# Optimization experiments

Measured on AMD Instinct MI355X. Metric: run time of the kernel, lower is better.

## Reference

```python
import jax, jax.numpy as jnp
import numpy as np

N_NODES = 100000
N_EDGES = 800000


def setup_inputs() -> dict:
    key = jax.random.key(0)
    ks = jax.random.split(key, 8)
    s = 0.05  # weight scale
    return {
        "x": jax.random.normal(ks[0], (N_NODES, 64), dtype=jnp.float32),
        "edge_index": jax.random.randint(ks[1], (2, N_EDGES), 0, N_NODES, dtype=jnp.int64),
        "eps1": jnp.zeros((), jnp.float32),
        "eps2": jnp.zeros((), jnp.float32),
        "W1a": jax.random.normal(ks[2], (64, 128), dtype=jnp.float32) * s,
        "b1a": jnp.zeros((128,), jnp.float32),
        "W1b": jax.random.normal(ks[3], (128, 128), dtype=jnp.float32) * s,
        "b1b": jnp.zeros((128,), jnp.float32),
        "W2a": jax.random.normal(ks[4], (128, 128), dtype=jnp.float32) * s,
        "b2a": jnp.zeros((128,), jnp.float32),
        "W2b": jax.random.normal(ks[5], (128, 64), dtype=jnp.float32) * s,
        "b2b": jnp.zeros((64,), jnp.float32),
    }


def _gin_conv(h, src, dst, eps, Wa, ba, Wb, bb, n_nodes):
    # sum-aggregate neighbor messages h[src] at dst, add (1+eps)*self
    agg = jax.ops.segment_sum(h[src], dst, num_segments=n_nodes)  # [N, d]
    z = (1.0 + eps) * h + agg
    # MLP: Linear -> ReLU -> Linear (weights stored [in, out])
    return jnp.maximum(z @ Wa + ba, 0.0) @ Wb + bb


def reference(x, edge_index, eps1, eps2, W1a, b1a, W1b, b1b, W2a, b2a, W2b, b2b):
    src, dst = edge_index[0], edge_index[1]
    n = x.shape[0]
    h = _gin_conv(x, src, dst, eps1, W1a, b1a, W1b, b1b, n)
    h = jnp.maximum(h, 0.0)  # outer ReLU; dropout is identity in eval
    out = _gin_conv(h, src, dst, eps2, W2a, b2a, W2b, b2b, n)
    return out
```

## Files before the change

kernel.cpp:

```cpp
#include <hip/hip_runtime.h>
#include <cstdint>

constexpr int CAP = 32;
constexpr int FIX = 16;

typedef __attribute__((ext_vector_type(8))) __bf16 bf16x8;
typedef __attribute__((ext_vector_type(16))) float f32x16;

__device__ __forceinline__ unsigned short f2bf(float f) {
    unsigned int u = __builtin_bit_cast(unsigned int, f);
    u += 0x7fffu + ((u >> 16) & 1u);
    return (unsigned short)(u >> 16);
}
__device__ __forceinline__ float bf2f(unsigned short h) {
    unsigned int u = ((unsigned int)h) << 16;
    return __builtin_bit_cast(float, u);
}


__global__ void init_kernel(int* __restrict__ counts, int N,
                            const float* __restrict__ W1a, const float* __restrict__ W1b,
                            const float* __restrict__ W2a, const float* __restrict__ W2b,
                            unsigned short* __restrict__ wpk) {
    int i = blockIdx.x * 256 + threadIdx.x;
    if (i < N) counts[i] = 0;
    if (i < 49152) {
        const float* W;
        int K, Nn, base, rel;
        if (i < 8192) {
            W = W1a; K = 64; Nn = 128; base = 0; rel = i;
        } else if (i < 24576) {
            W = W1b; K = 128; Nn = 128; base = 16384; rel = i - 8192;
        } else if (i < 40960) {
            W = W2a; K = 128; Nn = 128; base = 49152; rel = i - 24576;
        } else {
            W = W2b; K = 128; Nn = 64; base = 81920; rel = i - 40960;
        }
        int j = rel & 7;
        int lane = (rel >> 3) & 63;
        int rest = rel >> 9;
        int ksteps = K / 16;
        int kstep = rest % ksteps;
        int ntile = rest / ksteps;
        int k = kstep * 16 + ((lane >> 5) << 3) + j;
        int ncol = ntile * 32 + (lane & 31);
        float v = W[k * Nn + ncol];
        unsigned short h = f2bf(v);
        unsigned short l = f2bf(v - bf2f(h));
        wpk[base + rel] = h;
        wpk[base + K * Nn + rel] = l;
    }
}


__global__ void bucket_kernel(const int* __restrict__ eidx, int E,
                              int* __restrict__ counts, int* __restrict__ buckets) {
    int e = blockIdx.x * 256 + threadIdx.x;
    if (e < E) {
        int d = eidx[E + e];
        int pos = atomicAdd(&counts[d], 1);
        if (pos < CAP) buckets[(size_t)d * CAP + pos] = eidx[e];
    }
}


template <int KIN, int KMID, int KOUT, bool RELU_OUT>
__global__ __launch_bounds__(512, 8) void gin_layer_kernel(
    const float* __restrict__ h, const int* __restrict__ cnts, const int* __restrict__ buckets,
    const float* __restrict__ eps,
    const unsigned short* __restrict__ Wahi, const unsigned short* __restrict__ Walo,
    const float* __restrict__ ba,
    const unsigned short* __restrict__ Wbhi, const unsigned short* __restrict__ Wblo,
    const float* __restrict__ bb, float* __restrict__ out, int n) {
    constexpr int ZS = KIN + 8;
    constexpr int TS = KMID + 8;
    constexpr int KSB = KIN / 16;
    constexpr int KSC = KMID / 16;
    __shared__ __align__(16) unsigned short smem[2 * 64 * (KMID + 8)];
    unsigned short* const zhi = smem;
    unsigned short* const zlo = smem + 64 * ZS;
    unsigned short* const thi = smem;
    unsigned short* const tlo = smem + 64 * TS;

    const int tid = threadIdx.x;
    const int lane = tid & 63;
    const int base = blockIdx.x * 64;
    const float scale = 1.0f + eps[0];
    const int wq = __builtin_amdgcn_readfirstlane(tid >> 6);

    float h0x, h0y;
    if (KIN == 64) {
        h0x = h[lane];
        h0y = 0.f;
    } else {
        const float2* h2 = (const float2*)h;
        float2 t0 = h2[lane];
        h0x = t0.x;
        h0y = t0.y;
    }

#pragma unroll
    for (int mi = 0; mi < 8; ++mi) {
        const int m = wq * 8 + mi;
        const int node = base + m;
        const int nc = node < n ? node : n - 1;
        const int cl0 = __builtin_amdgcn_readfirstlane(cnts[nc]);
        const int cl = cl0 < CAP ? cl0 : CAP;
        const int* __restrict__ srcs = buckets + (size_t)nc * CAP;

        int sIdx[FIX];
#pragma unroll
        for (int j = 0; j < FIX; ++j) {
            int sj = srcs[j];
            sIdx[j] = j < cl ? sj : 0;
        }

        if (KIN == 64) {
            float a0 = 0.f, a1 = 0.f, a2 = 0.f, a3 = 0.f;
            float a4 = 0.f, a5 = 0.f, a6 = 0.f, a7 = 0.f;
#pragma unroll
            for (int j = 0; j < FIX; j += 8) {
                a0 += h[(size_t)sIdx[j + 0] * 64 + lane];
                a1 += h[(size_t)sIdx[j + 1] * 64 + lane];
                a2 += h[(size_t)sIdx[j + 2] * 64 + lane];
                a3 += h[(size_t)sIdx[j + 3] * 64 + lane];
                a4 += h[(size_t)sIdx[j + 4] * 64 + lane];
                a5 += h[(size_t)sIdx[j + 5] * 64 + lane];
                a6 += h[(size_t)sIdx[j + 6] * 64 + lane];
                a7 += h[(size_t)sIdx[j + 7] * 64 + lane];
            }
            float res = scale * h[(size_t)nc * 64 + lane];
            res += ((a0 + a1) + (a2 + a3)) + ((a4 + a5) + (a6 + a7));
            float corr = (float)(FIX - (cl < FIX ? cl : FIX));
            res = __builtin_fmaf(-corr, h0x, res);
            for (int e = FIX; e < cl; ++e) res += h[(size_t)srcs[e] * 64 + lane];
            unsigned short rh = f2bf(res);
            zhi[m * ZS + lane] = rh;
            zlo[m * ZS + lane] = f2bf(res - bf2f(rh));
        } else {
            const float2* h2 = (const float2*)h;
            float x0 = 0.f, x1 = 0.f, x2 = 0.f, x3 = 0.f;
            float y0 = 0.f, y1 = 0.f, y2 = 0.f, y3 = 0.f;
#pragma unroll
            for (int j = 0; j < FIX; j += 4) {
                float2 v0 = h2[(size_t)sIdx[j + 0] * 64 + lane];
                float2 v1 = h2[(size_t)sIdx[j + 1] * 64 + lane];
                float2 v2 = h2[(size_t)sIdx[j + 2] * 64 + lane];
                float2 v3 = h2[(size_t)sIdx[j + 3] * 64 + lane];
                x0 += v0.x;
                y0 += v0.y;
                x1 += v1.x;
                y1 += v1.y;
                x2 += v2.x;
                y2 += v2.y;
                x3 += v3.x;
                y3 += v3.y;
            }
            float2 a = h2[(size_t)nc * 64 + lane];
            float ax = scale * a.x + ((x0 + x1) + (x2 + x3));
            float ay = scale * a.y + ((y0 + y1) + (y2 + y3));
            float corr = (float)(FIX - (cl < FIX ? cl : FIX));
            ax = __builtin_fmaf(-corr, h0x, ax);
            ay = __builtin_fmaf(-corr, h0y, ay);
            for (int e = FIX; e < cl; ++e) {
                float2 v = h2[(size_t)srcs[e] * 64 + lane];
                ax += v.x;
                ay += v.y;
            }
            unsigned short hx = f2bf(ax), hy = f2bf(ay);
            unsigned short lx = f2bf(ax - bf2f(hx)), ly = f2bf(ay - bf2f(hy));
            *(unsigned int*)(zhi + m * ZS + 2 * lane) = (unsigned int)hx | ((unsigned int)hy << 16);
            *(unsigned int*)(zlo + m * ZS + 2 * lane) = (unsigned int)lx | ((unsigned int)ly << 16);
        }
    }
    __syncthreads();

    const int r31 = lane & 31;
    const int q = lane >> 5;

    {
        const int mt = wq & 1;
        const int nt = wq >> 1;
        f32x16 acc;
#pragma unroll
        for (int i = 0; i < 16; ++i) acc[i] = 0.0f;
        const unsigned short* Ah = zhi + (mt * 32 + r31) * ZS + q * 8;
        const unsigned short* Al = zlo + (mt * 32 + r31) * ZS + q * 8;
        const unsigned short* Bh = Wahi + ((size_t)(nt * KSB) * 64 + lane) * 8;
        const unsigned short* Bl = Walo + ((size_t)(nt * KSB) * 64 + lane) * 8;
#pragma unroll
        for (int ks = 0; ks < KSB; ++ks) {
            bf16x8 ah = *reinterpret_cast<const bf16x8*>(Ah + ks * 16);
            bf16x8 al = *reinterpret_cast<const bf16x8*>(Al + ks * 16);
            bf16x8 bh = *reinterpret_cast<const bf16x8*>(Bh + ks * 512);
            bf16x8 bl = *reinterpret_cast<const bf16x8*>(Bl + ks * 512);
            acc = __builtin_amdgcn_mfma_f32_32x32x16_bf16(ah, bh, acc, 0, 0, 0);
            acc = __builtin_amdgcn_mfma_f32_32x32x16_bf16(ah, bl, acc, 0, 0, 0);
            acc = __builtin_amdgcn_mfma_f32_32x32x16_bf16(al, bh, acc, 0, 0, 0);
        }
        const int col = nt * 32 + r31;
        const float bias = ba[col];
        unsigned short th_r[16], tl_r[16];
#pragma unroll
        for (int i = 0; i < 16; ++i) {
            float v = fmaxf(acc[i] + bias, 0.0f);
            unsigned short hh = f2bf(v);
            th_r[i] = hh;
            tl_r[i] = f2bf(v - bf2f(hh));
        }
        __syncthreads();
#pragma unroll
        for (int i = 0; i < 16; ++i) {
            const int m = mt * 32 + (i & 3) + 8 * (i >> 2) + 4 * q;
            thi[m * TS + col] = th_r[i];
            tlo[m * TS + col] = tl_r[i];
        }
    }
    __syncthreads();

    {
        constexpr int NKS = (KOUT == 64) ? (KSC / 2) : KSC;
        const int mt = wq & 1;
        const int nt = (KOUT == 64) ? ((wq >> 1) & 1) : (wq >> 1);
        const int k0 = (KOUT == 64) ? ((wq >> 2) * NKS) : 0;
        f32x16 acc;
#pragma unroll
        for (int i = 0; i < 16; ++i) acc[i] = 0.0f;
        const unsigned short* Ah = thi + (mt * 32 + r31) * TS + q * 8 + k0 * 16;
        const unsigned short* Al = tlo + (mt * 32 + r31) * TS + q * 8 + k0 * 16;
        const unsigned short* Bh = Wbhi + ((size_t)(nt * KSC + k0) * 64 + lane) * 8;
        const unsigned short* Bl = Wblo + ((size_t)(nt * KSC + k0) * 64 + lane) * 8;
#pragma unroll
        for (int ks = 0; ks < NKS; ++ks) {
            bf16x8 ah = *reinterpret_cast<const bf16x8*>(Ah + ks * 16);
            bf16x8 al = *reinterpret_cast<const bf16x8*>(Al + ks * 16);
            bf16x8 bh = *reinterpret_cast<const bf16x8*>(Bh + ks * 512);
            bf16x8 bl = *reinterpret_cast<const bf16x8*>(Bl + ks * 512);
            acc = __builtin_amdgcn_mfma_f32_32x32x16_bf16(ah, bh, acc, 0, 0, 0);
            acc = __builtin_amdgcn_mfma_f32_32x32x16_bf16(ah, bl, acc, 0, 0, 0);
            acc = __builtin_amdgcn_mfma_f32_32x32x16_bf16(al, bh, acc, 0, 0, 0);
        }
        const int col = nt * 32 + r31;
        if (KOUT == 64) {
            __syncthreads();
            float* stg = (float*)smem;
            if (wq >= 4) {
                float* d = stg + ((wq - 4) * 64 + lane) * 20;
#pragma unroll
                for (int c = 0; c < 4; ++c) {
                    float4 v = make_float4(acc[4 * c + 0], acc[4 * c + 1], acc[4 * c + 2],
                                           acc[4 * c + 3]);
                    *reinterpret_cast<float4*>(d + c * 4) = v;
                }
            }
            __syncthreads();
            if (wq < 4) {
                const float* s = stg + (wq * 64 + lane) * 20;
#pragma unroll
                for (int i = 0; i < 16; ++i) acc[i] += s[i];
                const float bias = bb[col];
#pragma unroll
                for (int i = 0; i < 16; ++i) {
                    const int m = mt * 32 + (i & 3) + 8 * (i >> 2) + 4 * q;
                    const int node = base + m;
                    if (node < n) {
                        float v = acc[i] + bias;
                        if (RELU_OUT) v = fmaxf(v, 0.0f);
                        out[(size_t)node * KOUT + col] = v;
                    }
                }
            }
        } else {
            const float bias = bb[col];
#pragma unroll
            for (int i = 0; i < 16; ++i) {
                const int m = mt * 32 + (i & 3) + 8 * (i >> 2) + 4 * q;
                const int node = base + m;
                if (node < n) {
                    float v = acc[i] + bias;
                    if (RELU_OUT) v = fmaxf(v, 0.0f);
                    out[(size_t)node * KOUT + col] = v;
                }
            }
        }
    }
}


extern "C" void kernel_launch(void* const* d_in, const int* in_sizes, int n_in,
                              void* d_out, int out_size, void* d_ws, size_t ws_size,
                              hipStream_t stream) {
    const float* x = (const float*)d_in[0];
    const int* eidx = (const int*)d_in[1];
    const float* eps1 = (const float*)d_in[2];
    const float* eps2 = (const float*)d_in[3];
    const float* W1a = (const float*)d_in[4];
    const float* b1a = (const float*)d_in[5];
    const float* W1b = (const float*)d_in[6];
    const float* b1b = (const float*)d_in[7];
    const float* W2a = (const float*)d_in[8];
    const float* b2a = (const float*)d_in[9];
    const float* W2b = (const float*)d_in[10];
    const float* b2b = (const float*)d_in[11];
    float* out = (float*)d_out;

    int N = in_sizes[0] / 64;
    int E = in_sizes[1] / 2;

    char* p = (char*)d_ws;
    auto alloc = [&](size_t bytes) {
        char* r = p;
        p += (bytes + 255) & ~(size_t)255;
        return r;
    };
    int* counts = (int*)alloc((size_t)N * 4);
    int* buckets = (int*)alloc((size_t)N * CAP * 4);
    float* h1 = (float*)alloc((size_t)N * 128 * 4);
    unsigned short* wpk = (unsigned short*)alloc(98304 * 2);

    int ib = ((N > 49152 ? N : 49152) + 255) / 256;
    int eb = (E + 255) / 256;
    int gb = (N + 63) / 64;

    init_kernel<<<ib, 256, 0, stream>>>(counts, N, W1a, W1b, W2a, W2b, wpk);
    bucket_kernel<<<eb, 256, 0, stream>>>(eidx, E, counts, buckets);

    gin_layer_kernel<64, 128, 128, true><<<gb, 512, 0, stream>>>(
        x, counts, buckets, eps1, wpk + 0, wpk + 8192, b1a, wpk + 16384, wpk + 32768, b1b, h1, N);
    gin_layer_kernel<128, 128, 64, false><<<gb, 512, 0, stream>>>(
        h1, counts, buckets, eps2, wpk + 49152, wpk + 65536, b2a, wpk + 81920, wpk + 90112, b2b,
        out, N);
}
```

Measured before the change: 271.4 us.

## Gather neighbor features in bf16 and store hidden layer as hi/lo bf16

Neighbor aggregation in both GIN layers now gathers only a bf16 copy of the node features. The goal is to roughly halve the random-gather memory traffic, which dominates the layers. The init kernel gains a pass converting x to bf16. Layer one writes its output as bf16 hi/lo halves, so the self term can still be rebuilt at near-fp32 precision while neighbors use only the hi half. The cost is an extra conversion pass over x and lower precision in the summed neighbor messages, which could push error toward the tolerance.

Result: faster. 246.2 us (-9.3%).

```diff
diff --git a/kernel.cpp b/kernel.cpp
--- a/kernel.cpp
+++ b/kernel.cpp
@@ -21,7 +21,8 @@
 __global__ void init_kernel(int* __restrict__ counts, int N,
                             const float* __restrict__ W1a, const float* __restrict__ W1b,
                             const float* __restrict__ W2a, const float* __restrict__ W2b,
-                            unsigned short* __restrict__ wpk) {
+                            unsigned short* __restrict__ wpk,
+                            const float* __restrict__ x, unsigned short* __restrict__ xbf) {
     int i = blockIdx.x * 256 + threadIdx.x;
     if (i < N) counts[i] = 0;
     if (i < 49152) {
@@ -50,6 +51,17 @@
         wpk[base + rel] = h;
         wpk[base + K * Nn + rel] = l;
     }
+    const int total4 = N * 16;
+    const int stride = gridDim.x * 256;
+    for (int t = i; t < total4; t += stride) {
+        float4 v = ((const float4*)x)[t];
+        ushort4 o;
+        o.x = f2bf(v.x);
+        o.y = f2bf(v.y);
+        o.z = f2bf(v.z);
+        o.w = f2bf(v.w);
+        ((ushort4*)xbf)[t] = o;
+    }
 }
 
 
@@ -64,14 +76,16 @@
 }
 
 
-template <int KIN, int KMID, int KOUT, bool RELU_OUT>
+template <int KIN, int KMID, int KOUT, bool RELU_OUT, bool SELF_F32, bool BF_OUT>
 __global__ __launch_bounds__(512, 8) void gin_layer_kernel(
-    const float* __restrict__ h, const int* __restrict__ cnts, const int* __restrict__ buckets,
-    const float* __restrict__ eps,
+    const unsigned short* __restrict__ ghi, const unsigned short* __restrict__ glo,
+    const float* __restrict__ hf32, const int* __restrict__ cnts,
+    const int* __restrict__ buckets, const float* __restrict__ eps,
     const unsigned short* __restrict__ Wahi, const unsigned short* __restrict__ Walo,
     const float* __restrict__ ba,
     const unsigned short* __restrict__ Wbhi, const unsigned short* __restrict__ Wblo,
-    const float* __restrict__ bb, float* __restrict__ out, int n) {
+    const float* __restrict__ bb, float* __restrict__ out_f32,
+    unsigned short* __restrict__ outhi, unsigned short* __restrict__ outlo, int n) {
     constexpr int ZS = KIN + 8;
     constexpr int TS = KMID + 8;
     constexpr int KSB = KIN / 16;
@@ -90,13 +104,12 @@
 
     float h0x, h0y;
     if (KIN == 64) {
-        h0x = h[lane];
+        h0x = bf2f(ghi[lane]);
         h0y = 0.f;
     } else {
-        const float2* h2 = (const float2*)h;
-        float2 t0 = h2[lane];
-        h0x = t0.x;
-        h0y = t0.y;
+        unsigned int u0 = ((const unsigned int*)ghi)[lane];
+        h0x = bf2f((unsigned short)(u0 & 0xffffu));
+        h0y = bf2f((unsigned short)(u0 >> 16));
     }
 
 #pragma unroll
@@ -120,52 +133,70 @@
             float a4 = 0.f, a5 = 0.f, a6 = 0.f, a7 = 0.f;
 #pragma unroll
             for (int j = 0; j < FIX; j += 8) {
-                a0 += h[(size_t)sIdx[j + 0] * 64 + lane];
-                a1 += h[(size_t)sIdx[j + 1] * 64 + lane];
-                a2 += h[(size_t)sIdx[j + 2] * 64 + lane];
-                a3 += h[(size_t)sIdx[j + 3] * 64 + lane];
-                a4 += h[(size_t)sIdx[j + 4] * 64 + lane];
-                a5 += h[(size_t)sIdx[j + 5] * 64 + lane];
-                a6 += h[(size_t)sIdx[j + 6] * 64 + lane];
-                a7 += h[(size_t)sIdx[j + 7] * 64 + lane];
-            }
-            float res = scale * h[(size_t)nc * 64 + lane];
+                a0 += bf2f(ghi[(size_t)sIdx[j + 0] * 64 + lane]);
+                a1 += bf2f(ghi[(size_t)sIdx[j + 1] * 64 + lane]);
+                a2 += bf2f(ghi[(size_t)sIdx[j + 2] * 64 + lane]);
+                a3 += bf2f(ghi[(size_t)sIdx[j + 3] * 64 + lane]);
+                a4 += bf2f(ghi[(size_t)sIdx[j + 4] * 64 + lane]);
+                a5 += bf2f(ghi[(size_t)sIdx[j + 5] * 64 + lane]);
+                a6 += bf2f(ghi[(size_t)sIdx[j + 6] * 64 + lane]);
+                a7 += bf2f(ghi[(size_t)sIdx[j + 7] * 64 + lane]);
+            }
+            float self;
+            if (SELF_F32) {
+                self = hf32[(size_t)nc * 64 + lane];
+            } else {
+                self = bf2f(ghi[(size_t)nc * 64 + lane]) + bf2f(glo[(size_t)nc * 64 + lane]);
+            }
+            float res = scale * self;
             res += ((a0 + a1) + (a2 + a3)) + ((a4 + a5) + (a6 + a7));
             float corr = (float)(FIX - (cl < FIX ? cl : FIX));
             res = __builtin_fmaf(-corr, h0x, res);
-            for (int e = FIX; e < cl; ++e) res += h[(size_t)srcs[e] * 64 + lane];
+            for (int e = FIX; e < cl; ++e)
+                res += bf2f(ghi[(size_t)srcs[e] * 64 + lane]);
             unsigned short rh = f2bf(res);
             zhi[m * ZS + lane] = rh;
             zlo[m * ZS + lane] = f2bf(res - bf2f(rh));
         } else {
-            const float2* h2 = (const float2*)h;
+            const unsigned int* g32 = (const unsigned int*)ghi;
             float x0 = 0.f, x1 = 0.f, x2 = 0.f, x3 = 0.f;
             float y0 = 0.f, y1 = 0.f, y2 = 0.f, y3 = 0.f;
 #pragma unroll
             for (int j = 0; j < FIX; j += 4) {
-                float2 v0 = h2[(size_t)sIdx[j + 0] * 64 + lane];
-                float2 v1 = h2[(size_t)sIdx[j + 1] * 64 + lane];
-                float2 v2 = h2[(size_t)sIdx[j + 2] * 64 + lane];
-                float2 v3 = h2[(size_t)sIdx[j + 3] * 64 + lane];
-                x0 += v0.x;
-                y0 += v0.y;
-                x1 += v1.x;
-                y1 += v1.y;
-                x2 += v2.x;
-                y2 += v2.y;
-                x3 += v3.x;
-                y3 += v3.y;
-            }
-            float2 a = h2[(size_t)nc * 64 + lane];
-            float ax = scale * a.x + ((x0 + x1) + (x2 + x3));
-            float ay = scale * a.y + ((y0 + y1) + (y2 + y3));
+                unsigned int v0 = g32[(size_t)sIdx[j + 0] * 64 + lane];
+                unsigned int v1 = g32[(size_t)sIdx[j + 1] * 64 + lane];
+                unsigned int v2 = g32[(size_t)sIdx[j + 2] * 64 + lane];
+                unsigned int v3 = g32[(size_t)sIdx[j + 3] * 64 + lane];
+                x0 += bf2f((unsigned short)(v0 & 0xffffu));
+                y0 += bf2f((unsigned short)(v0 >> 16));
+                x1 += bf2f((unsigned short)(v1 & 0xffffu));
+                y1 += bf2f((unsigned short)(v1 >> 16));
+                x2 += bf2f((unsigned short)(v2 & 0xffffu));
+                y2 += bf2f((unsigned short)(v2 >> 16));
+                x3 += bf2f((unsigned short)(v3 & 0xffffu));
+                y3 += bf2f((unsigned short)(v3 >> 16));
+            }
+            float sx, sy;
+            if (SELF_F32) {
+                const float2* h2 = (const float2*)hf32;
+                float2 a = h2[(size_t)nc * 64 + lane];
+                sx = a.x;
+                sy = a.y;
+            } else {
+                unsigned int sh = g32[(size_t)nc * 64 + lane];
+                unsigned int sl = ((const unsigned int*)glo)[(size_t)nc * 64 + lane];
+                sx = bf2f((unsigned short)(sh & 0xffffu)) + bf2f((unsigned short)(sl & 0xffffu));
+                sy = bf2f((unsigned short)(sh >> 16)) + bf2f((unsigned short)(sl >> 16));
+            }
+            float ax = scale * sx + ((x0 + x1) + (x2 + x3));
+            float ay = scale * sy + ((y0 + y1) + (y2 + y3));
             float corr = (float)(FIX - (cl < FIX ? cl : FIX));
             ax = __builtin_fmaf(-corr, h0x, ax);
             ay = __builtin_fmaf(-corr, h0y, ay);
             for (int e = FIX; e < cl; ++e) {
-                float2 v = h2[(size_t)srcs[e] * 64 + lane];
-                ax += v.x;
-                ay += v.y;
+                unsigned int v = g32[(size_t)srcs[e] * 64 + lane];
+                ax += bf2f((unsigned short)(v & 0xffffu));
+                ay += bf2f((unsigned short)(v >> 16));
             }
             unsigned short hx = f2bf(ax), hy = f2bf(ay);
             unsigned short lx = f2bf(ax - bf2f(hx)), ly = f2bf(ay - bf2f(hy));
@@ -266,7 +297,7 @@
                     if (node < n) {
                         float v = acc[i] + bias;
                         if (RELU_OUT) v = fmaxf(v, 0.0f);
-                        out[(size_t)node * KOUT + col] = v;
+                        out_f32[(size_t)node * KOUT + col] = v;
                     }
                 }
             }
@@ -279,7 +310,13 @@
                 if (node < n) {
                     float v = acc[i] + bias;
                     if (RELU_OUT) v = fmaxf(v, 0.0f);
-                    out[(size_t)node * KOUT + col] = v;
+                    if (BF_OUT) {
+                        unsigned short hh = f2bf(v);
+                        outhi[(size_t)node * KOUT + col] = hh;
+                        outlo[(size_t)node * KOUT + col] = f2bf(v - bf2f(hh));
+                    } else {
+                        out_f32[(size_t)node * KOUT + col] = v;
+                    }
                 }
             }
         }
@@ -315,19 +352,22 @@
     };
     int* counts = (int*)alloc((size_t)N * 4);
     int* buckets = (int*)alloc((size_t)N * CAP * 4);
-    float* h1 = (float*)alloc((size_t)N * 128 * 4);
+    unsigned short* h1hi = (unsigned short*)alloc((size_t)N * 128 * 2);
+    unsigned short* h1lo = (unsigned short*)alloc((size_t)N * 128 * 2);
+    unsigned short* xbf = (unsigned short*)alloc((size_t)N * 64 * 2);
     unsigned short* wpk = (unsigned short*)alloc(98304 * 2);
 
     int ib = ((N > 49152 ? N : 49152) + 255) / 256;
     int eb = (E + 255) / 256;
     int gb = (N + 63) / 64;
 
-    init_kernel<<<ib, 256, 0, stream>>>(counts, N, W1a, W1b, W2a, W2b, wpk);
+    init_kernel<<<ib, 256, 0, stream>>>(counts, N, W1a, W1b, W2a, W2b, wpk, x, xbf);
     bucket_kernel<<<eb, 256, 0, stream>>>(eidx, E, counts, buckets);
 
-    gin_layer_kernel<64, 128, 128, true><<<gb, 512, 0, stream>>>(
-        x, counts, buckets, eps1, wpk + 0, wpk + 8192, b1a, wpk + 16384, wpk + 32768, b1b, h1, N);
-    gin_layer_kernel<128, 128, 64, false><<<gb, 512, 0, stream>>>(
-        h1, counts, buckets, eps2, wpk + 49152, wpk + 65536, b2a, wpk + 81920, wpk + 90112, b2b,
-        out, N);
-}
+    gin_layer_kernel<64, 128, 128, true, true, true><<<gb, 512, 0, stream>>>(
+        xbf, (const unsigned short*)nullptr, x, counts, buckets, eps1, wpk + 0, wpk + 8192, b1a,
+        wpk + 16384, wpk + 32768, b1b, (float*)nullptr, h1hi, h1lo, N);
+    gin_layer_kernel<128, 128, 64, false, false, false><<<gb, 512, 0, stream>>>(
+        h1hi, h1lo, (const float*)nullptr, counts, buckets, eps2, wpk + 49152, wpk + 65536, b2a,
+        wpk + 81920, wpk + 90112, b2b, out, (unsigned short*)nullptr, (unsigned short*)nullptr, N);
+}
```
